# Kernel tuning notes

Measured on AMD Instinct MI355X. Metric: run time of the kernel, lower is better.

## Reference

```python
import jax, jax.numpy as jnp
import numpy as np
import math

EPS_BN1 = 1e-3   # batch_norm1 eps
EPS_BNP = 1e-5   # predictor BN default eps


def conv1d(x, w, b=None, stride=1, padding=0, dilation=1):
    # x: (B, Cin, T), w: (Cout, Cin, K)
    out = jax.lax.conv_general_dilated(
        x, w, window_strides=(stride,), padding=[(padding, padding)],
        rhs_dilation=(dilation,), dimension_numbers=('NCH', 'OIH', 'NCH'))
    if b is not None:
        out = out + b[None, :, None]
    return out


def bn_eval(x, g, b, m, v, eps):
    scale = g / jnp.sqrt(v + eps)
    return (x - m[None, :, None]) * scale[None, :, None] + b[None, :, None]


def setup_inputs() -> dict:
    key = jax.random.key(0)
    ks = jax.random.split(key, 16)
    B, Cin, T = 16, 256, 4096
    Cout, P = 256, 32
    f32 = jnp.float32

    def n(k, shape, s):
        return s * jax.random.normal(k, shape, dtype=f32)

    inp = {
        'x': n(ks[0], (B, Cin, T), 1.0),
        'conv1_w': n(ks[1], (2 * Cout, Cin, 1), 0.06),
        'bn1_g': 1.0 + n(ks[2], (2 * Cout,), 0.1),
        'bn1_b': n(ks[3], (2 * Cout,), 0.1),
        'bn1_m': n(ks[4], (2 * Cout,), 0.1),
        'bn1_v': 1.0 + 0.1 * jax.random.uniform(ks[5], (2 * Cout,), dtype=f32),
        'conv1x1_w': n(ks[6], (1, Cin, 1), 0.06),
        'p0_w': n(ks[7], (P, 2, 31), 0.1),
        'p0_b': n(ks[8], (P,), 0.05),
        'p0bn_g': jnp.ones((P,), f32), 'p0bn_b': jnp.zeros((P,), f32),
        'p0bn_m': n(ks[9], (P,), 0.1),
        'p0bn_v': 1.0 + 0.1 * jax.random.uniform(ks[10], (P,), dtype=f32),
        'p1_w': n(ks[11], (P, P, 15), 0.05),
        'p1_b': n(ks[12], (P,), 0.05),
        'p1bn_g': jnp.ones((P,), f32), 'p1bn_b': jnp.zeros((P,), f32),
        'p1bn_m': n(ks[13], (P,), 0.1),
        'p1bn_v': 1.0 + 0.1 * jax.random.uniform(ks[14], (P,), dtype=f32),
        # last predictor conv: weight scaled by 0.01, bias = -log(2) (per __init__)
        'p2_w': 0.01 * n(ks[15], (2, P, 15), 0.05),
        'p2_b': jnp.array([-math.log(2.0), -math.log(2.0)], dtype=f32),
        'norm_mean': jnp.ones((1,), f32),  # registered buffer, eval renorm
    }
    return inp


def _forward(x, conv1_w, bn1_g, bn1_b, bn1_m, bn1_v, conv1x1_w,
             p0_w, p0_b, p0bn_g, p0bn_b, p0bn_m, p0bn_v,
             p1_w, p1_b, p1bn_g, p1bn_b, p1bn_m, p1bn_v,
             p2_w, p2_b, norm_mean):
    B, Cin, T = x.shape
    sg = jax.lax.stop_gradient

    # conv1 -> BN -> GLU(dim=1); dropout is identity in eval
    feat = bn_eval(conv1d(x, conv1_w), bn1_g, bn1_b, bn1_m, bn1_v, EPS_BN1)
    a, g = jnp.split(feat, 2, axis=1)
    feat = a * jax.nn.sigmoid(g)                     # (B, Cout, T)

    # predictor on [__x, __x^2]
    xx = conv1d(x, conv1x1_w)                        # (B, 1, T)
    h = jnp.concatenate([xx, xx * xx], axis=1)       # (B, 2, T)
    h = jax.nn.silu(bn_eval(conv1d(h, p0_w, p0_b, padding=15),
                            p0bn_g, p0bn_b, p0bn_m, p0bn_v, EPS_BNP))
    h = jax.nn.silu(bn_eval(conv1d(h, p1_w, p1_b, padding=7),
                            p1bn_g, p1bn_b, p1bn_m, p1bn_v, EPS_BNP))
    jumps = conv1d(h, p2_w, p2_b, padding=7)         # (B, 2, T)

    weights = jax.nn.sigmoid(jumps[:, 0, :])         # (B, T)
    moves = jax.nn.sigmoid(jumps[:, 1, :]) * norm_mean[0]  # eval: renorm = norm_mean
    row_renorm = jnp.maximum(jnp.mean(moves, axis=1), 1.0)
    moves = moves / row_renorm[:, None]

    features = jnp.transpose(feat, (0, 2, 1))        # (B, T, C)
    fw = features * weights[:, :, None]

    # big_pool: poses value = cumsum(moves); grad path = local window of 21 moves
    # (the k=1..20 shift loop adds grad-only terms). Window sum via cumsum diff.
    c = jnp.cumsum(moves, axis=1)
    win = c - jnp.pad(c, ((0, 0), (21, 0)))[:, :T]   # sum of moves[i-20..i]
    poses = sg(c) + win - sg(win)                    # (B, T)

    floors = jnp.floor(poses)
    ceils = floors + 1.0
    w1 = 1.0 - (poses - floors)                      # func = line: 1 - t
    w2 = 1.0 - (ceils - poses)

    # moves <= 1 (sigmoid * norm_mean=1 / row_renorm>=1) => ceils.max()+1 <= T+2
    L = T + 2                                        # static bound for out length
    C = features.shape[2]
    bidx = jnp.arange(B)[:, None]
    fi = floors.astype(jnp.int32)
    ci = fi + 1
    out = jnp.zeros((B, L, C), dtype=features.dtype)
    out = out.at[bidx, fi].add(w1[:, :, None] * fw)
    out = out.at[bidx, ci].add(w2[:, :, None] * fw)

    x_evs = jnp.transpose(out, (0, 2, 1))            # (B, C, L)
    pad = 15 - (L % 15)                              # F.pad(0, 15 - L % 15)
    return jnp.pad(x_evs, ((0, 0), (0, 0), (0, pad)))


def reference(x, conv1_w, bn1_g, bn1_b, bn1_m, bn1_v, conv1x1_w,
              p0_w, p0_b, p0bn_g, p0bn_b, p0bn_m, p0bn_v,
              p1_w, p1_b, p1bn_g, p1bn_b, p1bn_m, p1bn_v,
              p2_w, p2_b, norm_mean):
    return _forward(x, conv1_w, bn1_g, bn1_b, bn1_m, bn1_v, conv1x1_w,
                    p0_w, p0_b, p0bn_g, p0bn_b, p0bn_m, p0bn_v,
                    p1_w, p1_b, p1bn_g, p1bn_b, p1bn_m, p1bn_v,
                    p2_w, p2_b, norm_mean)
```

## Files before the change

### kernel.cpp

```cpp
#include <hip/hip_runtime.h>
#include <hip/hip_bf16.h>

#define BB   16
#define CIN  256
#define TN   4096
#define LOUT 4110
#define FTS  4224

typedef __attribute__((ext_vector_type(8))) short s16x8;
typedef __attribute__((ext_vector_type(4))) float f32x4;

__device__ __forceinline__ float fsig(float g) {
  return __builtin_amdgcn_rcpf(1.f + __expf(-g));
}


__global__ __launch_bounds__(256) void k0_prep(
    const float* __restrict__ conv1_w, const float* __restrict__ p0_w,
    const float* __restrict__ p1_w, const float* __restrict__ p2_w,
    const float* __restrict__ bn1_g, const float* __restrict__ bn1_b,
    const float* __restrict__ bn1_m, const float* __restrict__ bn1_v,
    const float* __restrict__ p0_b, const float* __restrict__ p0g,
    const float* __restrict__ p0bb, const float* __restrict__ p0m,
    const float* __restrict__ p0v,
    const float* __restrict__ p1_b, const float* __restrict__ p1g,
    const float* __restrict__ p1bb, const float* __restrict__ p1m,
    const float* __restrict__ p1v,
    short* __restrict__ wBpk, float4* __restrict__ bnp,
    float* __restrict__ wp0T, short* __restrict__ wp1M,
    short* __restrict__ wp2M, float2* __restrict__ bnp0,
    float2* __restrict__ bnp1) {
  int bid = blockIdx.x, tid = threadIdx.x;
  if (bid < 512) {
    int e = bid * 256 + tid;
    int i = e & 7, l = (e >> 3) & 63, ks = (e >> 9) & 7, n16 = e >> 12;
    int n = n16 * 16 + (l & 15);
    int j = n & 63;
    int co = (j < 32) ? ((n >> 6) * 32 + j) : (256 + (n >> 6) * 32 + (j - 32));
    int ci = ks * 32 + (l >> 4) * 8 + i;
    __hip_bfloat16 hv = __float2bfloat16(conv1_w[co * 256 + ci]);
    wBpk[e] = *(short*)&hv;
  } else {
    int idx = (bid - 512) * 256 + tid;
    if (idx < 1984) {
      int ch = idx & 31, rem = idx >> 5;
      int ic = rem / 31, k = rem % 31;
      wp0T[idx] = p0_w[(ch * 2 + ic) * 31 + k];
    }
    {
      int i = idx & 7, l = (idx >> 3) & 63, nf = (idx >> 9) & 1, koff = idx >> 10;
      int ch = nf * 16 + (l & 15), ic = (l >> 4) * 8 + i;
      __hip_bfloat16 hv = __float2bfloat16(p1_w[(ch * 32 + ic) * 15 + koff]);
      wp1M[idx] = *(short*)&hv;
    }
    if (idx < 7680) {
      int i = idx & 7, l = (idx >> 3) & 63, koff = idx >> 9;
      int n = l & 15, ic = (l >> 4) * 8 + i;
      float v = (n < 2) ? p2_w[(n * 32 + ic) * 15 + koff] : 0.f;
      __hip_bfloat16 hv = __float2bfloat16(v);
      wp2M[idx] = *(short*)&hv;
    }
    if (idx < 32) {
      int ch = idx;
      float sc = p0g[ch] * rsqrtf(p0v[ch] + 1e-5f);
      bnp0[ch] = make_float2(sc, (p0_b[ch] - p0m[ch]) * sc + p0bb[ch]);
    }
    if (idx >= 32 && idx < 64) {
      int ch = idx - 32;
      float sc = p1g[ch] * rsqrtf(p1v[ch] + 1e-5f);
      bnp1[ch] = make_float2(sc, (p1_b[ch] - p1m[ch]) * sc + p1bb[ch]);
    }
    if (idx < 256) {
      int c = idx;
      float sa = bn1_g[c] * rsqrtf(bn1_v[c] + 1e-3f);
      float ba = bn1_b[c] - bn1_m[c] * sa;
      float sg = bn1_g[c + 256] * rsqrtf(bn1_v[c + 256] + 1e-3f);
      float bg = bn1_b[c + 256] - bn1_m[c + 256] * sg;
      bnp[c] = make_float4(sa, ba, sg, bg);
    }
  }
}

__global__ __launch_bounds__(256, 8) void k1_mfma(
    const float* __restrict__ x, const float* __restrict__ w1x1,
    const short* __restrict__ wBpk, const float4* __restrict__ bnp,
    __hip_bfloat16* __restrict__ featT, float* __restrict__ xx) {
  int bid = blockIdx.x;
  int xcd = bid & 7, kk = bid >> 3;
  int nblk = kk & 3;
  int T = (kk >> 2) * 8 + xcd;
  int ty = T & 127, b = T >> 7;
  int t0 = ty * 32;
  __shared__ __align__(16) unsigned int hb[32 * 132];
  __shared__ float xws[4][36];
  int tid = threadIdx.x;
  int l = tid & 63, wv = tid >> 6;
  int tg = l & 7, Ch = l >> 3;
  int q = (tg >> 1) & 3;
  const float* xb = x + (size_t)b * (CIN * TN) + t0 + 4 * tg;
  float xxp[4] = {0.f, 0.f, 0.f, 0.f};
#pragma unroll
  for (int iter = 0; iter < 4; ++iter) {
    int C = Ch + 8 * wv + 32 * iter;
    int ci = 2 * C;
    float4 f0 = *(const float4*)(xb + (size_t)ci * TN);
    float4 f1 = *(const float4*)(xb + (size_t)(ci + 1) * TN);
    float w0 = w1x1[ci], w1 = w1x1[ci + 1];
    unsigned int* dst = hb + (C ^ (q << 2));
    float fa[4] = {f0.x, f0.y, f0.z, f0.w};
    float fb[4] = {f1.x, f1.y, f1.z, f1.w};
#pragma unroll
    for (int r = 0; r < 4; ++r) {
      __hip_bfloat16 lo = __float2bfloat16(fa[r]);
      __hip_bfloat16 hi = __float2bfloat16(fb[r]);
      unsigned int pk = (unsigned int)(*(unsigned short*)&lo) |
                        ((unsigned int)(*(unsigned short*)&hi) << 16);
      dst[(4 * tg + r) * 132] = pk;
      xxp[r] = fmaf(w0, fa[r], fmaf(w1, fb[r], xxp[r]));
    }
  }
#pragma unroll
  for (int r = 0; r < 4; ++r) {
    xxp[r] += __shfl_xor(xxp[r], 8);
    xxp[r] += __shfl_xor(xxp[r], 16);
    xxp[r] += __shfl_xor(xxp[r], 32);
  }
  if (l < 8) {
#pragma unroll
    for (int r = 0; r < 4; ++r) xws[wv][4 * l + r] = xxp[r];
  }

  int lr = l & 15, lk = l >> 4;
  int glu = 2 * nblk + (wv >> 1), sub = wv & 1;
  int n16a = glu * 4 + sub;
  const short* wrow = wBpk + (size_t)l * 8;
  s16x8 bf0 = *(const s16x8*)(wrow + (size_t)n16a * 4096);
  s16x8 bf1 = *(const s16x8*)(wrow + (size_t)(n16a + 2) * 4096);

  __syncthreads();
  if (tid < 32)
    xx[b * TN + t0 + tid] = xws[0][tid] + xws[1][tid] + xws[2][tid] + xws[3][tid];

  f32x4 acc[2][2];
#pragma unroll
  for (int i = 0; i < 2; ++i) {
    acc[i][0] = (f32x4){0.f, 0.f, 0.f, 0.f};
    acc[i][1] = (f32x4){0.f, 0.f, 0.f, 0.f};
  }

#pragma unroll
  for (int ks = 0; ks < 8; ++ks) {
    s16x8 af[2];
#pragma unroll
    for (int mf = 0; mf < 2; ++mf) {
      int row = mf * 16 + lr;
      int grp = ks * 4 + lk;
      int qr = (row >> 3) & 3;
      af[mf] = *(const s16x8*)(hb + row * 132 + ((grp ^ qr) << 2));
    }
    s16x8 nbf0, nbf1;
    if (ks < 7) {
      nbf0 = *(const s16x8*)(wrow + (size_t)n16a * 4096 + (ks + 1) * 512);
      nbf1 = *(const s16x8*)(wrow + (size_t)(n16a + 2) * 4096 + (ks + 1) * 512);
    }
#pragma unroll
    for (int mf = 0; mf < 2; ++mf) {
      acc[mf][0] = __builtin_amdgcn_mfma_f32_16x16x32_bf16(af[mf], bf0, acc[mf][0], 0, 0, 0);
      acc[mf][1] = __builtin_amdgcn_mfma_f32_16x16x32_bf16(af[mf], bf1, acc[mf][1], 0, 0, 0);
    }
    if (ks < 7) { bf0 = nbf0; bf1 = nbf1; }
  }

  int c = glu * 32 + sub * 16 + lr;
  float4 bn = bnp[c];
#pragma unroll
  for (int mf = 0; mf < 2; ++mf) {
#pragma unroll
    for (int r = 0; r < 4; ++r) {
      float a = acc[mf][0][r], g = acc[mf][1][r];
      float av = fmaf(a, bn.x, bn.y);
      float gv = fmaf(g, bn.z, bn.w);
      float fv = av * fsig(gv);
      int t = t0 + mf * 16 + lk * 4 + r;
      featT[((size_t)b * TN + t) * 256 + c] = __float2bfloat16(fv);
    }
  }
}

__global__ __launch_bounds__(512) void k2_pred(
    const float* __restrict__ xx,
    const float* __restrict__ wp0T, const float2* __restrict__ bnp0,
    const short* __restrict__ wp1M, const float2* __restrict__ bnp1,
    const short* __restrict__ wp2M, const float* __restrict__ p2_b,
    const float* __restrict__ norm_mean,
    float* __restrict__ wts, float* __restrict__ mvr) {
  int t0 = blockIdx.x * 128;
  int b = blockIdx.y;
  __shared__ float xin[2][192];
  __shared__ short h0T[160 * 40];
  __shared__ short h1T[144 * 40];
  int tid = threadIdx.x;
  for (int q = tid; q < 192; q += 512) {
    int t = t0 - 29 + q;
    float v = (q < 186 && t >= 0 && t < TN) ? xx[b * TN + t] : 0.f;
    xin[0][q] = v;
    xin[1][q] = v * v;
  }
  __syncthreads();
  {
    int ch = tid & 31, tq = tid >> 5;
    int i0 = tq * 12;
    if (i0 < 156) {
      float2 bb0 = bnp0[ch];
      float a0[12];
#pragma unroll
      for (int j = 0; j < 12; ++j) a0[j] = 0.f;
#pragma unroll
      for (int ic = 0; ic < 2; ++ic) {
        float rr[44];
#pragma unroll
        for (int q = 0; q < 11; ++q) {
          float4 t4 = *(const float4*)(&xin[ic][i0 + q * 4]);
          rr[q * 4 + 0] = t4.x; rr[q * 4 + 1] = t4.y;
          rr[q * 4 + 2] = t4.z; rr[q * 4 + 3] = t4.w;
        }
#pragma unroll
        for (int k = 0; k < 31; ++k) {
          float w = wp0T[(ic * 31 + k) * 32 + ch];
#pragma unroll
          for (int j = 0; j < 12; ++j) a0[j] = fmaf(w, rr[j + k], a0[j]);
        }
      }
#pragma unroll
      for (int j = 0; j < 12; ++j) {
        int i = i0 + j;
        if (i < 156) {
          float v = a0[j] * bb0.x + bb0.y;
          float h = v * fsig(v);
          __hip_bfloat16 hv = __float2bfloat16(h);
          h0T[i * 40 + ch] = *(short*)&hv;
        }
      }
    }
    if (tid < 128) h0T[(156 + (tid >> 5)) * 40 + (tid & 31)] = 0;
  }
  __syncthreads();
  int l = tid & 63, wv = tid >> 6;
  int lrow = l & 15, lk8 = (l >> 4) * 8;
  {
    f32x4 acc[2][2];
#pragma unroll
    for (int i = 0; i < 2; ++i)
#pragma unroll
      for (int j = 0; j < 2; ++j) acc[i][j] = (f32x4){0.f, 0.f, 0.f, 0.f};
    int nmf = (wv == 0) ? 2 : 1;
    for (int koff = 0; koff < 15; ++koff) {
      const short* bp = wp1M + koff * 1024;
      s16x8 bf0 = *(const s16x8*)(bp + l * 8);
      s16x8 bf1 = *(const s16x8*)(bp + 512 + l * 8);
      for (int mi = 0; mi < nmf; ++mi) {
        int mf = (mi == 0) ? wv : 8;
        s16x8 af = *(const s16x8*)(&h0T[(mf * 16 + koff + lrow) * 40 + lk8]);
        acc[mi][0] = __builtin_amdgcn_mfma_f32_16x16x32_bf16(af, bf0, acc[mi][0], 0, 0, 0);
        acc[mi][1] = __builtin_amdgcn_mfma_f32_16x16x32_bf16(af, bf1, acc[mi][1], 0, 0, 0);
      }
    }
    for (int mi = 0; mi < nmf; ++mi) {
      int mf = (mi == 0) ? wv : 8;
#pragma unroll
      for (int nf = 0; nf < 2; ++nf) {
        int ch = nf * 16 + lrow;
        float2 bb = bnp1[ch];
#pragma unroll
        for (int r = 0; r < 4; ++r) {
          int row = mf * 16 + (l >> 4) * 4 + r;
          float v = acc[mi][nf][r] * bb.x + bb.y;
          float h = v * fsig(v);
          __hip_bfloat16 hv = __float2bfloat16(h);
          h1T[row * 40 + ch] = *(short*)&hv;
        }
      }
    }
  }
  __syncthreads();
  {
    f32x4 acc2 = (f32x4){0.f, 0.f, 0.f, 0.f};
    for (int koff = 0; koff < 15; ++koff) {
      s16x8 bf = *(const s16x8*)(wp2M + koff * 512 + l * 8);
      s16x8 af = *(const s16x8*)(&h1T[(wv * 16 + koff + lrow) * 40 + lk8]);
      acc2 = __builtin_amdgcn_mfma_f32_16x16x32_bf16(af, bf, acc2, 0, 0, 0);
    }
    int ch = lrow;
    if (ch < 2) {
      float pb = p2_b[ch];
      float nm = norm_mean[0];
#pragma unroll
      for (int r = 0; r < 4; ++r) {
        int t = t0 + wv * 16 + (l >> 4) * 4 + r;
        float a = acc2[r] + pb;
        float s = fsig(a);
        if (ch == 0) wts[b * TN + t] = s;
        else         mvr[b * TN + t] = s * nm;
      }
    }
  }
}

__global__ __launch_bounds__(256) void k3_scan(const float* __restrict__ mvr,
                                               float* __restrict__ poses,
                                               int* __restrict__ firstT) {
  int b = blockIdx.x, tid = threadIdx.x;
  __shared__ float csum[256];
  __shared__ int shlast;
  float v[16];
  const float* src = mvr + b * TN + tid * 16;
  float run = 0.f;
#pragma unroll
  for (int j = 0; j < 16; ++j) { run += src[j]; v[j] = run; }
  csum[tid] = run;
  __syncthreads();
  for (int off = 1; off < 256; off <<= 1) {
    float tv = (tid >= off) ? csum[tid - off] : 0.f;
    __syncthreads();
    csum[tid] += tv;
    __syncthreads();
  }
  float incl = csum[tid];
  float total = csum[255];
  float excl = incl - run;
  __syncthreads();
  float rn = total * (1.0f / 4096.0f);
  float inv = (rn > 1.0f) ? 1.0f / rn : 1.0f;
  float p16[16];
  float* pd = poses + b * TN + tid * 16;
#pragma unroll
  for (int j = 0; j < 16; ++j) { p16[j] = (excl + v[j]) * inv; pd[j] = p16[j]; }
  csum[tid] = p16[15];
  __syncthreads();
  int* ft = firstT + b * FTS;
  int prevf = (tid == 0) ? -1 : min((int)floorf(csum[tid - 1]), 4220);
  int f = prevf;
#pragma unroll
  for (int j = 0; j < 16; ++j) {
    f = min((int)floorf(p16[j]), 4220);
    for (int l = prevf + 1; l <= f; ++l) ft[l] = tid * 16 + j;
    prevf = f;
  }
  if (tid == 255) shlast = f;
  __syncthreads();
  for (int l = shlast + 1 + tid; l < FTS; l += 256) ft[l] = TN;
}

__global__ __launch_bounds__(256) void k4_gather(
    const __hip_bfloat16* __restrict__ featT, const float* __restrict__ wts,
    const float* __restrict__ poses, const int* __restrict__ firstT,
    float* __restrict__ out) {
  int d = blockIdx.x + 257 * blockIdx.y;
  int w = (d & 7) * 514 + (d >> 3);
  int lx = w % 257, b = w / 257;
  int l0 = lx * 16;
  __shared__ float acc[16][259];
  int tid = threadIdx.x;
  for (int i = tid; i < 16 * 259; i += 256) ((float*)acc)[i] = 0.f;
  const int* ft = firstT + b * FTS;
  int ts = (l0 == 0) ? 0 : ft[l0 - 1];
  int te = ft[l0 + 16];
  __syncthreads();
  int c = tid;
  if (ts < te) {
    const float* pp = poses + b * TN;
    const float* wp = wts + b * TN;
    const __hip_bfloat16* fp = featT + (size_t)(b * TN) * 256 + c;
    float p_cur = pp[ts];
    float w_cur = wp[ts];
    float f_cur = __bfloat162float(fp[(size_t)ts * 256]);
    float S_lo = 0.f, S_hi = 0.f;
    int cur = (int)floorf(p_cur);
    for (int t = ts; t < te; ++t) {
      float p_nxt = 0.f, w_nxt = 0.f, f_nxt = 0.f;
      if (t + 1 < te) {
        p_nxt = pp[t + 1];
        w_nxt = wp[t + 1];
        f_nxt = __bfloat162float(fp[(size_t)(t + 1) * 256]);
      }
      int fi = (int)floorf(p_cur);
      if (fi < cur) fi = cur;
      if (fi != cur) {
        int r = cur - l0;
        if (r >= 0 && r < 16) acc[r][c] = S_lo;
        if (fi == cur + 1) {
          S_lo = S_hi;
        } else {
          int r2 = cur + 1 - l0;
          if (r2 >= 0 && r2 < 16) acc[r2][c] = S_hi;
          S_lo = 0.f;
        }
        S_hi = 0.f;
        cur = fi;
      }
      float w2 = p_cur - (float)fi;
      float fw = f_cur * w_cur;
      S_lo = fmaf(1.f - w2, fw, S_lo);
      S_hi = fmaf(w2, fw, S_hi);
      p_cur = p_nxt; w_cur = w_nxt; f_cur = f_nxt;
    }
    int r = cur - l0;
    if (r >= 0 && r < 16) acc[r][c] = S_lo;
    int r2 = cur + 1 - l0;
    if (r2 >= 0 && r2 < 16) acc[r2][c] = S_hi;
  }
  __syncthreads();
  for (int i = tid; i < 4096; i += 256) {
    int c2 = i >> 4, r = i & 15;
    int l = l0 + r;
    if (l < LOUT) out[((size_t)b * 256 + c2) * LOUT + l] = acc[r][c2];
  }
}

extern "C" void kernel_launch(void* const* d_in, const int* in_sizes, int n_in,
                              void* d_out, int out_size, void* d_ws, size_t ws_size,
                              hipStream_t stream) {
  const float* x       = (const float*)d_in[0];
  const float* conv1_w = (const float*)d_in[1];
  const float* bn1_g   = (const float*)d_in[2];
  const float* bn1_b   = (const float*)d_in[3];
  const float* bn1_m   = (const float*)d_in[4];
  const float* bn1_v   = (const float*)d_in[5];
  const float* w1x1    = (const float*)d_in[6];
  const float* p0_w    = (const float*)d_in[7];
  const float* p0_b    = (const float*)d_in[8];
  const float* p0g     = (const float*)d_in[9];
  const float* p0bb    = (const float*)d_in[10];
  const float* p0m     = (const float*)d_in[11];
  const float* p0v     = (const float*)d_in[12];
  const float* p1_w    = (const float*)d_in[13];
  const float* p1_b    = (const float*)d_in[14];
  const float* p1g     = (const float*)d_in[15];
  const float* p1bb    = (const float*)d_in[16];
  const float* p1m     = (const float*)d_in[17];
  const float* p1v     = (const float*)d_in[18];
  const float* p2_w    = (const float*)d_in[19];
  const float* p2_b    = (const float*)d_in[20];
  const float* nmean   = (const float*)d_in[21];

  char* ws = (char*)d_ws;
  __hip_bfloat16* featT = (__hip_bfloat16*)ws;
  short* wBpk   = (short*)(ws + 33554432);
  float4* bnp   = (float4*)(ws + 33816576);
  float* wp0T   = (float*)(ws + 33820672);
  short* wp1M   = (short*)(ws + 33828864);
  short* wp2M   = (short*)(ws + 33859584);
  float2* bnp0  = (float2*)(ws + 33874944);
  float2* bnp1  = (float2*)(ws + 33875200);
  float* xx     = (float*)(ws + 33890304);
  float* wts    = (float*)(ws + 34152448);
  float* mvr    = (float*)(ws + 34414592);
  float* poses  = (float*)(ws + 34676736);
  int*   firstT = (int*)  (ws + 34938880);
  float* out    = (float*)d_out;

  k0_prep<<<dim3(572), dim3(256), 0, stream>>>(
      conv1_w, p0_w, p1_w, p2_w, bn1_g, bn1_b, bn1_m, bn1_v,
      p0_b, p0g, p0bb, p0m, p0v, p1_b, p1g, p1bb, p1m, p1v,
      wBpk, bnp, wp0T, wp1M, wp2M, bnp0, bnp1);
  k1_mfma<<<dim3(8192), dim3(256), 0, stream>>>(x, w1x1, wBpk, bnp, featT, xx);
  k2_pred<<<dim3(32, 16), dim3(512), 0, stream>>>(xx, wp0T, bnp0, wp1M, bnp1,
                                                  wp2M, p2_b, nmean, wts, mvr);
  k3_scan<<<dim3(16), dim3(256), 0, stream>>>(mvr, poses, firstT);
  k4_gather<<<dim3(257, 16), dim3(256), 0, stream>>>(featT, wts, poses, firstT, out);
}
```

Baseline: 98.50 us.

## Make k1 blocks persistent over four time tiles with weights held in registers

Each k1 block now processes four consecutive 32-step time tiles instead of one, so the grid shrinks from 8192 to 2048 blocks. The full per-wave B-fragment weight slice (8x2 vectors) is loaded into registers once and reused across all four tiles, which removes repeated global weight loads and block launch overhead. The cost is higher register pressure (launch bounds relaxed from 8 to 4 blocks per CU), an extra barrier per tile, and no overlap between the x load of one tile and the MFMA work of the previous one.

```diff
diff --git a/kernel.cpp b/kernel.cpp
--- a/kernel.cpp
+++ b/kernel.cpp
@@ -81,108 +81,109 @@
   }
 }
 
-__global__ __launch_bounds__(256, 8) void k1_mfma(
+__global__ __launch_bounds__(256, 4) void k1_mfma(
     const float* __restrict__ x, const float* __restrict__ w1x1,
     const short* __restrict__ wBpk, const float4* __restrict__ bnp,
     __hip_bfloat16* __restrict__ featT, float* __restrict__ xx) {
   int bid = blockIdx.x;
-  int xcd = bid & 7, kk = bid >> 3;
-  int nblk = kk & 3;
-  int T = (kk >> 2) * 8 + xcd;
-  int ty = T & 127, b = T >> 7;
-  int t0 = ty * 32;
+  int xcd = bid & 7, r_ = bid >> 3;
+  int nblk = r_ & 3;
+  int span_id = (r_ >> 2) * 8 + xcd;
+  int b = span_id >> 5;
+  int t_base = (span_id & 31) * 128;
   __shared__ __align__(16) unsigned int hb[32 * 132];
   __shared__ float xws[4][36];
   int tid = threadIdx.x;
   int l = tid & 63, wv = tid >> 6;
   int tg = l & 7, Ch = l >> 3;
   int q = (tg >> 1) & 3;
-  const float* xb = x + (size_t)b * (CIN * TN) + t0 + 4 * tg;
-  float xxp[4] = {0.f, 0.f, 0.f, 0.f};
-#pragma unroll
-  for (int iter = 0; iter < 4; ++iter) {
-    int C = Ch + 8 * wv + 32 * iter;
-    int ci = 2 * C;
-    float4 f0 = *(const float4*)(xb + (size_t)ci * TN);
-    float4 f1 = *(const float4*)(xb + (size_t)(ci + 1) * TN);
-    float w0 = w1x1[ci], w1 = w1x1[ci + 1];
-    unsigned int* dst = hb + (C ^ (q << 2));
-    float fa[4] = {f0.x, f0.y, f0.z, f0.w};
-    float fb[4] = {f1.x, f1.y, f1.z, f1.w};
-#pragma unroll
-    for (int r = 0; r < 4; ++r) {
-      __hip_bfloat16 lo = __float2bfloat16(fa[r]);
-      __hip_bfloat16 hi = __float2bfloat16(fb[r]);
-      unsigned int pk = (unsigned int)(*(unsigned short*)&lo) |
-                        ((unsigned int)(*(unsigned short*)&hi) << 16);
-      dst[(4 * tg + r) * 132] = pk;
-      xxp[r] = fmaf(w0, fa[r], fmaf(w1, fb[r], xxp[r]));
-    }
-  }
-#pragma unroll
-  for (int r = 0; r < 4; ++r) {
-    xxp[r] += __shfl_xor(xxp[r], 8);
-    xxp[r] += __shfl_xor(xxp[r], 16);
-    xxp[r] += __shfl_xor(xxp[r], 32);
-  }
-  if (l < 8) {
-#pragma unroll
-    for (int r = 0; r < 4; ++r) xws[wv][4 * l + r] = xxp[r];
-  }
-
   int lr = l & 15, lk = l >> 4;
   int glu = 2 * nblk + (wv >> 1), sub = wv & 1;
   int n16a = glu * 4 + sub;
   const short* wrow = wBpk + (size_t)l * 8;
-  s16x8 bf0 = *(const s16x8*)(wrow + (size_t)n16a * 4096);
-  s16x8 bf1 = *(const s16x8*)(wrow + (size_t)(n16a + 2) * 4096);
-
-  __syncthreads();
-  if (tid < 32)
-    xx[b * TN + t0 + tid] = xws[0][tid] + xws[1][tid] + xws[2][tid] + xws[3][tid];
-
-  f32x4 acc[2][2];
-#pragma unroll
-  for (int i = 0; i < 2; ++i) {
-    acc[i][0] = (f32x4){0.f, 0.f, 0.f, 0.f};
-    acc[i][1] = (f32x4){0.f, 0.f, 0.f, 0.f};
-  }
-
+
+  s16x8 breg[8][2];
 #pragma unroll
   for (int ks = 0; ks < 8; ++ks) {
-    s16x8 af[2];
-#pragma unroll
-    for (int mf = 0; mf < 2; ++mf) {
-      int row = mf * 16 + lr;
-      int grp = ks * 4 + lk;
-      int qr = (row >> 3) & 3;
-      af[mf] = *(const s16x8*)(hb + row * 132 + ((grp ^ qr) << 2));
-    }
-    s16x8 nbf0, nbf1;
-    if (ks < 7) {
-      nbf0 = *(const s16x8*)(wrow + (size_t)n16a * 4096 + (ks + 1) * 512);
-      nbf1 = *(const s16x8*)(wrow + (size_t)(n16a + 2) * 4096 + (ks + 1) * 512);
-    }
-#pragma unroll
-    for (int mf = 0; mf < 2; ++mf) {
-      acc[mf][0] = __builtin_amdgcn_mfma_f32_16x16x32_bf16(af[mf], bf0, acc[mf][0], 0, 0, 0);
-      acc[mf][1] = __builtin_amdgcn_mfma_f32_16x16x32_bf16(af[mf], bf1, acc[mf][1], 0, 0, 0);
-    }
-    if (ks < 7) { bf0 = nbf0; bf1 = nbf1; }
-  }
-
+    breg[ks][0] = *(const s16x8*)(wrow + (size_t)n16a * 4096 + ks * 512);
+    breg[ks][1] = *(const s16x8*)(wrow + (size_t)(n16a + 2) * 4096 + ks * 512);
+  }
   int c = glu * 32 + sub * 16 + lr;
   float4 bn = bnp[c];
-#pragma unroll
-  for (int mf = 0; mf < 2; ++mf) {
-#pragma unroll
-    for (int r = 0; r < 4; ++r) {
-      float a = acc[mf][0][r], g = acc[mf][1][r];
-      float av = fmaf(a, bn.x, bn.y);
-      float gv = fmaf(g, bn.z, bn.w);
-      float fv = av * fsig(gv);
-      int t = t0 + mf * 16 + lk * 4 + r;
-      featT[((size_t)b * TN + t) * 256 + c] = __float2bfloat16(fv);
+
+  for (int s4 = 0; s4 < 4; ++s4) {
+    int t0 = t_base + s4 * 32;
+    if (s4) __syncthreads();
+    const float* xb = x + (size_t)b * (CIN * TN) + t0 + 4 * tg;
+    float xxp[4] = {0.f, 0.f, 0.f, 0.f};
+#pragma unroll
+    for (int iter = 0; iter < 4; ++iter) {
+      int C = Ch + 8 * wv + 32 * iter;
+      int ci = 2 * C;
+      float4 f0 = *(const float4*)(xb + (size_t)ci * TN);
+      float4 f1 = *(const float4*)(xb + (size_t)(ci + 1) * TN);
+      float w0 = w1x1[ci], w1 = w1x1[ci + 1];
+      unsigned int* dst = hb + (C ^ (q << 2));
+      float fa[4] = {f0.x, f0.y, f0.z, f0.w};
+      float fb[4] = {f1.x, f1.y, f1.z, f1.w};
+#pragma unroll
+      for (int rr = 0; rr < 4; ++rr) {
+        __hip_bfloat16 lo = __float2bfloat16(fa[rr]);
+        __hip_bfloat16 hi = __float2bfloat16(fb[rr]);
+        unsigned int pk = (unsigned int)(*(unsigned short*)&lo) |
+                          ((unsigned int)(*(unsigned short*)&hi) << 16);
+        dst[(4 * tg + rr) * 132] = pk;
+        xxp[rr] = fmaf(w0, fa[rr], fmaf(w1, fb[rr], xxp[rr]));
+      }
+    }
+#pragma unroll
+    for (int rr = 0; rr < 4; ++rr) {
+      xxp[rr] += __shfl_xor(xxp[rr], 8);
+      xxp[rr] += __shfl_xor(xxp[rr], 16);
+      xxp[rr] += __shfl_xor(xxp[rr], 32);
+    }
+    if (l < 8) {
+#pragma unroll
+      for (int rr = 0; rr < 4; ++rr) xws[wv][4 * l + rr] = xxp[rr];
+    }
+    __syncthreads();
+    if (tid < 32)
+      xx[b * TN + t0 + tid] = xws[0][tid] + xws[1][tid] + xws[2][tid] + xws[3][tid];
+
+    f32x4 acc[2][2];
+#pragma unroll
+    for (int i = 0; i < 2; ++i) {
+      acc[i][0] = (f32x4){0.f, 0.f, 0.f, 0.f};
+      acc[i][1] = (f32x4){0.f, 0.f, 0.f, 0.f};
+    }
+#pragma unroll
+    for (int ks = 0; ks < 8; ++ks) {
+      s16x8 af[2];
+#pragma unroll
+      for (int mf = 0; mf < 2; ++mf) {
+        int row = mf * 16 + lr;
+        int grp = ks * 4 + lk;
+        int qr = (row >> 3) & 3;
+        af[mf] = *(const s16x8*)(hb + row * 132 + ((grp ^ qr) << 2));
+      }
+#pragma unroll
+      for (int mf = 0; mf < 2; ++mf) {
+        acc[mf][0] = __builtin_amdgcn_mfma_f32_16x16x32_bf16(af[mf], breg[ks][0], acc[mf][0], 0, 0, 0);
+        acc[mf][1] = __builtin_amdgcn_mfma_f32_16x16x32_bf16(af[mf], breg[ks][1], acc[mf][1], 0, 0, 0);
+      }
+    }
+
+#pragma unroll
+    for (int mf = 0; mf < 2; ++mf) {
+#pragma unroll
+      for (int rr = 0; rr < 4; ++rr) {
+        float a = acc[mf][0][rr], g = acc[mf][1][rr];
+        float av = fmaf(a, bn.x, bn.y);
+        float gv = fmaf(g, bn.z, bn.w);
+        float fv = av * fsig(gv);
+        int t = t0 + mf * 16 + lk * 4 + rr;
+        featT[((size_t)b * TN + t) * 256 + c] = __float2bfloat16(fv);
+      }
     }
   }
 }
@@ -463,7 +464,7 @@
       conv1_w, p0_w, p1_w, p2_w, bn1_g, bn1_b, bn1_m, bn1_v,
       p0_b, p0g, p0bb, p0m, p0v, p1_b, p1g, p1bb, p1m, p1v,
       wBpk, bnp, wp0T, wp1M, wp2M, bnp0, bnp1);
-  k1_mfma<<<dim3(8192), dim3(256), 0, stream>>>(x, w1x1, wBpk, bnp, featT, xx);
+  k1_mfma<<<dim3(2048), dim3(256), 0, stream>>>(x, w1x1, wBpk, bnp, featT, xx);
   k2_pred<<<dim3(32, 16), dim3(512), 0, stream>>>(xx, wp0T, bnp0, wp1M, bnp1,
                                                   wp2M, p2_b, nmean, wts, mvr);
   k3_scan<<<dim3(16), dim3(256), 0, stream>>>(mvr, poses, firstT);
```

Result: slower. 123.6 us (+25.4%).
